# Performance work log

Measured on AMD Instinct MI355X. Metric: run time of the kernel, lower is better.

Reference implementation:

```python
import jax, jax.numpy as jnp
import numpy as np

IS, OS, H = 168, 24, 256           # input window, output horizon, state_hsize
TAU, MAXIMUM = 0.1, 1.0            # tau parameter (non-grad) and series maximum
DILS = [[1, 4], [16, 64]]          # ResidualDRNN groups of dilations


def _lstm(x, wih, whh, bih, bhh):
    """Single-layer LSTM over time-major x: (T, B, C). PyTorch gate order i,f,g,o."""
    def step(carry, xt):
        h, c = carry
        g = xt @ wih.T + h @ whh.T + (bih + bhh)
        i, f, gg, o = jnp.split(g, 4, axis=-1)
        c = jax.nn.sigmoid(f) * c + jax.nn.sigmoid(i) * jnp.tanh(gg)
        h = jax.nn.sigmoid(o) * jnp.tanh(c)
        return (h, c), h
    h0 = jnp.zeros((x.shape[1], H), x.dtype)
    _, hs = jax.lax.scan(step, (h0, h0), x)
    return hs


def _dilated_lstm(x, d, p):
    """Standard DRNN layer: pad T to multiple of d, interleave time into batch, run LSTM."""
    T, B, C = x.shape
    n = -(-T // d)
    xp = jnp.pad(x, ((0, n * d - T), (0, 0), (0, 0)))
    hd = _lstm(xp.reshape(n, d * B, C), *p)
    return hd.reshape(n * d, B, H)[:T]


def _forward(train, init_lev_sm, lstm_params, nl_w, nl_b, sc_w, sc_b):
    B, T = train.shape
    a = jax.nn.sigmoid(init_lev_sm[0])            # lev_sms (idxs are all 0 -> same scalar)
    floor = TAU * MAXIMUM                          # tau * maximum
    # --- exponential-smoothing level recurrence (sequential) ---
    lev0 = jnp.maximum(train[:, 0], floor)
    def step(lev, xt):
        new = jnp.maximum(a * xt + (1.0 - a) * lev, floor)
        return new, new
    _, rest = jax.lax.scan(step, lev0, train[:, 1:].T)
    levs = jnp.concatenate([lev0[None], rest], axis=0).T   # [B, T]
    # --- windowed normalization ---
    w_idx = jnp.arange(IS - 1, T)                           # W = T - IS + 1 window ends
    in_win = train[:, (w_idx - IS + 1)[:, None] + jnp.arange(IS)[None, :]]
    in_win = (in_win / levs[:, w_idx][:, :, None]).transpose(1, 0, 2)    # [W, B, IS]
    o_idx = jnp.arange(IS - 1, T - OS)                      # W_out = T - OS - IS + 1
    out_win = train[:, (o_idx + 1)[:, None] + jnp.arange(OS)[None, :]]
    out_win = (out_win / levs[:, o_idx][:, :, None]).transpose(1, 0, 2)  # [W_out, B, OS]
    # --- ResidualDRNN stack on window_input[:-OS] (time-major: windows are the sequence) ---
    x = in_win[:-OS]
    li = 0
    for g, dils in enumerate(DILS):
        residual = x
        h = x
        for d in dils:
            h = _dilated_lstm(h, d, lstm_params[li])
            li += 1
        x = h + residual if g > 0 else h                    # dropout p=0 -> identity
    x = jnp.tanh(x @ nl_w.T + nl_b)                         # add_nl_layer
    pred = x @ sc_w.T + sc_b                                # scoring
    return pred, out_win


def setup_inputs() -> dict:
    key = jax.random.key(0)
    ks = list(jax.random.split(key, 32))
    B, T = 32, 1024
    inp = {
        "train": jax.random.uniform(ks[0], (B, T), jnp.float32, 0.05, 1.0),
        "val": jax.random.uniform(ks[1], (B, T), jnp.float32, 0.05, 1.0),
        "test": jax.random.uniform(ks[2], (B, T), jnp.float32, 0.05, 1.0),
        "idxs": jnp.zeros((B,), jnp.int32),
        "init_lev_sm": jnp.array([0.5], jnp.float32),
    }
    sizes = [IS, H, H, H]  # input feature size of each of the 4 DRNN layers
    k = 3
    s = 1.0 / np.sqrt(H)
    for i, cin in enumerate(sizes):
        inp[f"wih{i}"] = jax.random.uniform(ks[k], (4 * H, cin), jnp.float32, -s, s); k += 1
        inp[f"whh{i}"] = jax.random.uniform(ks[k], (4 * H, H), jnp.float32, -s, s); k += 1
        inp[f"bih{i}"] = jax.random.uniform(ks[k], (4 * H,), jnp.float32, -s, s); k += 1
        inp[f"bhh{i}"] = jax.random.uniform(ks[k], (4 * H,), jnp.float32, -s, s); k += 1
    inp["nl_w"] = jax.random.uniform(ks[k], (H, H), jnp.float32, -s, s); k += 1
    inp["nl_b"] = jnp.zeros((H,), jnp.float32)
    inp["sc_w"] = jax.random.uniform(ks[k], (OS, H), jnp.float32, -s, s); k += 1
    inp["sc_b"] = jnp.zeros((OS,), jnp.float32)
    return inp


def reference(train, val, test, idxs, init_lev_sm,
              wih0, whh0, bih0, bhh0, wih1, whh1, bih1, bhh1,
              wih2, whh2, bih2, bhh2, wih3, whh3, bih3, bhh3,
              nl_w, nl_b, sc_w, sc_b):
    lstm_params = [(wih0, whh0, bih0, bhh0), (wih1, whh1, bih1, bhh1),
                   (wih2, whh2, bih2, bhh2), (wih3, whh3, bih3, bhh3)]
    # training path (validating=False, testing=False): only `train` is used
    return _forward(train, init_lev_sm, lstm_params, nl_w, nl_b, sc_w, sc_b)
```

## Files before the change

kernel.cpp:

```cpp
#include <hip/hip_runtime.h>
#include <hip/hip_fp16.h>
#include <math.h>

#define TT 833
#define GDIM 1024

typedef _Float16 f16x8 __attribute__((ext_vector_type(8)));
typedef float    f32x4 __attribute__((ext_vector_type(4)));

#if __has_builtin(__builtin_amdgcn_rcpf)
__device__ __forceinline__ float frcp(float x){ return __builtin_amdgcn_rcpf(x); }
#else
__device__ __forceinline__ float frcp(float x){ return 1.f/x; }
#endif

#if __has_builtin(__builtin_amdgcn_sdot4)
__device__ __forceinline__ int sdot4(unsigned a, unsigned b, int c){
  return __builtin_amdgcn_sdot4((int)a, (int)b, c, false);
}
#else
__device__ __forceinline__ int sdot4(unsigned a, unsigned b, int c){
  int ai = (int)a, bi = (int)b;
  c += ((ai<<24)>>24)*((bi<<24)>>24);
  c += ((ai<<16)>>24)*((bi<<16)>>24);
  c += ((ai<<8)>>24)*((bi<<8)>>24);
  c += (ai>>24)*(bi>>24);
  return c;
}
#endif

__device__ __forceinline__ void lds_barrier(){
  asm volatile("s_waitcnt lgkmcnt(0)" ::: "memory");
  __builtin_amdgcn_s_barrier();
  __builtin_amdgcn_sched_barrier(0);
}


__global__ void levels_k(const float* __restrict__ train, const float* __restrict__ ism,
                         float* __restrict__ levs){
  int b = threadIdx.x;
  if (b >= 32) return;
  float a = 1.f/(1.f+expf(-ism[0]));
  const float4* tr4 = reinterpret_cast<const float4*>(train + b*1024);
  float4* lv4 = reinterpret_cast<float4*>(levs + b*1024);
  float lev = 0.f;
  for (int i = 0; i < 256; ++i){
    float4 v = tr4[i];
    float4 o;
    if (i == 0) o.x = lev = fmaxf(v.x, 0.1f);
    else        o.x = lev = fmaxf(fmaf(a, v.x, (1.f-a)*lev), 0.1f);
    o.y = lev = fmaxf(fmaf(a, v.y, (1.f-a)*lev), 0.1f);
    o.z = lev = fmaxf(fmaf(a, v.z, (1.f-a)*lev), 0.1f);
    o.w = lev = fmaxf(fmaf(a, v.w, (1.f-a)*lev), 0.1f);
    lv4[i] = o;
  }
}

__global__ void win_x_k(const float* __restrict__ train, const float* __restrict__ levs,
                        __half* __restrict__ x0){
  int idx = blockIdx.x*256 + threadIdx.x;
  int i = idx % 168;
  int r = idx / 168;
  int b = r & 31;
  int t = r >> 5;
  x0[idx] = __float2half(train[b*1024 + t + i] / levs[b*1024 + t + 167]);
}

__global__ void win_out_k(const float* __restrict__ train, const float* __restrict__ levs,
                          float* __restrict__ ow){
  int idx = blockIdx.x*256 + threadIdx.x;
  int o = idx % 24;
  int r = idx / 24;
  int b = r & 31;
  int t = r >> 5;
  ow[idx] = train[b*1024 + 168 + t + o] / levs[b*1024 + t + 167];
}

__global__ void permw_k(const float* __restrict__ wih, const float* __restrict__ bih,
                        const float* __restrict__ bhh, __half* __restrict__ wP,
                        float* __restrict__ bP, int K){
  int t = blockIdx.x;
  int g = ((t & 3) << 8) + (t >> 2);
  for (int k = threadIdx.x; k < K; k += 256)
    wP[(size_t)t*K + k] = __float2half(wih[(size_t)g*K + k]);
  if (threadIdx.x == 0) bP[t] = bih[g] + bhh[g];
}

__global__ void cvth_k(const float* __restrict__ s, __half* __restrict__ d, int n){
  int i = blockIdx.x*256 + threadIdx.x;
  if (i < n) d[i] = __float2half(s[i]);
}

__global__ void packq_k(const float* __restrict__ w, uint4* __restrict__ wq,
                        float* __restrict__ sc){
  int t = blockIdx.x*256 + threadIdx.x;
  if (t >= 1024) return;
  int g = ((t & 3) << 8) + (t >> 2);
  const float* row = w + (size_t)g*256;
  float amax = 0.f;
  for (int k = 0; k < 256; ++k) amax = fmaxf(amax, fabsf(row[k]));
  amax = fmaxf(amax, 1e-20f);
  float s = amax/127.f, inv = 127.f/amax;
  sc[t] = s;
  for (int k16 = 0; k16 < 16; ++k16){
    union { uint4 u; signed char b[16]; } r;
    #pragma unroll
    for (int j = 0; j < 16; ++j){
      float q = rintf(row[k16*16 + j]*inv);
      q = fminf(fmaxf(q, -127.f), 127.f);
      r.b[j] = (signed char)q;
    }
    wq[(size_t)k16*1024 + t] = r.u;
  }
}

__global__ __launch_bounds__(256) void proj_mfma(
    const _Float16* __restrict__ A, const _Float16* __restrict__ W,
    const float* __restrict__ b1,
    void* __restrict__ C, int Mout, int K, int N, int dil, int act, int outHalf)
{
  __shared__ _Float16 As[128*40];
  __shared__ _Float16 Bs[128*40];
  const int tid = threadIdx.x;
  const int lane = tid & 63;
  const int w = tid >> 6, wr = w >> 1, wc = w & 1;
  const int m0 = blockIdx.y << 7, n0 = blockIdx.x << 7;

  const int rowA = tid >> 1;
  int srcrow;
  {
    int m = m0 + rowA;
    if (dil == 0) srcrow = (m < Mout) ? m : -1;
    else {
      int rows = dil << 5;
      int j = m / rows;
      int q = m - j*rows;
      int t = j*dil + (q >> 5);
      srcrow = (t < TT) ? ((t << 5) + (q & 31)) : -1;
    }
  }
  const int halfsel = tid & 1;
  const int nrow = n0 + rowA;

  f32x4 acc[4][4];
  #pragma unroll
  for (int i = 0; i < 4; ++i)
    #pragma unroll
    for (int j = 0; j < 4; ++j) acc[i][j] = (f32x4){0.f,0.f,0.f,0.f};

  const int nkt = (K + 31) >> 5;
  for (int kt = 0; kt < nkt; ++kt){
    const int k0 = (kt << 5) + halfsel*16;
    {
      union { uint4 u[2]; _Float16 h[16]; } tmp;
      if (srcrow >= 0 && k0 + 16 <= K){
        const uint4* s = reinterpret_cast<const uint4*>(A + (size_t)srcrow*K + k0);
        tmp.u[0] = s[0]; tmp.u[1] = s[1];
      } else {
        const _Float16* s = (srcrow >= 0) ? A + (size_t)srcrow*K : nullptr;
        #pragma unroll
        for (int j = 0; j < 16; ++j){
          int kk = k0 + j;
          tmp.h[j] = (s && kk < K) ? s[kk] : (_Float16)0.f;
        }
      }
      uint4* dst = reinterpret_cast<uint4*>(&As[rowA*40 + halfsel*16]);
      dst[0] = tmp.u[0]; dst[1] = tmp.u[1];
    }
    {
      union { uint4 u[2]; _Float16 h[16]; } tmp;
      if (k0 + 16 <= K){
        const uint4* s = reinterpret_cast<const uint4*>(W + (size_t)nrow*K + k0);
        tmp.u[0] = s[0]; tmp.u[1] = s[1];
      } else {
        const _Float16* s = W + (size_t)nrow*K;
        #pragma unroll
        for (int j = 0; j < 16; ++j){
          int kk = k0 + j;
          tmp.h[j] = (kk < K) ? s[kk] : (_Float16)0.f;
        }
      }
      uint4* dst = reinterpret_cast<uint4*>(&Bs[rowA*40 + halfsel*16]);
      dst[0] = tmp.u[0]; dst[1] = tmp.u[1];
    }
    __syncthreads();
    {
      const int kg = lane >> 4, r16 = lane & 15;
      f16x8 af[4], bf[4];
      #pragma unroll
      for (int mi = 0; mi < 4; ++mi)
        af[mi] = *reinterpret_cast<const f16x8*>(&As[(wr*64 + mi*16 + r16)*40 + kg*8]);
      #pragma unroll
      for (int nj = 0; nj < 4; ++nj)
        bf[nj] = *reinterpret_cast<const f16x8*>(&Bs[(wc*64 + nj*16 + r16)*40 + kg*8]);
      #pragma unroll
      for (int mi = 0; mi < 4; ++mi)
        #pragma unroll
        for (int nj = 0; nj < 4; ++nj)
          acc[mi][nj] = __builtin_amdgcn_mfma_f32_16x16x32_f16(af[mi], bf[nj], acc[mi][nj], 0, 0, 0);
    }
    __syncthreads();
  }
  #pragma unroll
  for (int mi = 0; mi < 4; ++mi){
    #pragma unroll
    for (int p = 0; p < 4; ++p){
      int mrow = m0 + wr*64 + mi*16 + (lane >> 4)*4 + p;
      if (mrow >= Mout) continue;
      #pragma unroll
      for (int nj = 0; nj < 4; ++nj){
        int ncol = n0 + wc*64 + nj*16 + (lane & 15);
        float v = acc[mi][nj][p] + b1[ncol];
        if (act) v = tanhf(v);
        if (outHalf) reinterpret_cast<__half*>(C)[(size_t)mrow*N + ncol] = __float2half(v);
        else reinterpret_cast<float*>(C)[(size_t)mrow*N + ncol] = v;
      }
    }
  }
}

template<int NR>
__global__ __launch_bounds__(512, 1) void srecr2_k(
    const uint4* __restrict__ wq, const float* __restrict__ scale,
    const __half* __restrict__ Gin,
    __half* __restrict__ outh, float* __restrict__ outf,
    int nsteps, int d, int rowsTotal)
{
  __shared__ __align__(16) unsigned int hq[2][NR][64];
  const int tid = threadIdx.x;
  const int s = tid & 1;
  const int j = tid >> 1;
  const int q0 = blockIdx.x*NR;
  const float sg0 = scale[2*tid]*(1.f/127.f);
  const float sg1 = scale[2*tid + 1]*(1.f/127.f);
  uint4 w0_[16], w1_[16];
  #pragma unroll
  for (int kk = 0; kk < 16; ++kk){
    w0_[kk] = wq[(size_t)kk*1024 + 2*tid];
    w1_[kk] = wq[(size_t)kk*1024 + 2*tid + 1];
  }
  float c[NR];
  #pragma unroll
  for (int rr = 0; rr < NR; ++rr) c[rr] = 0.f;
  for (int e = tid; e < 2*NR*64; e += 512) (&hq[0][0][0])[e] = 0u;
  __syncthreads();

  for (int step = 0; step < nsteps; ++step){
    const int cur = step & 1;
    const __half2* gbase = reinterpret_cast<const __half2*>(
        Gin + ((size_t)step*rowsTotal + q0)*GDIM);
    #pragma unroll
    for (int rr = 0; rr < NR; ++rr){
      __half2 g2 = gbase[rr*512 + tid];
      float gin0 = __half2float(__low2half(g2));
      float gin1 = __half2float(__high2half(g2));
      int a00 = 0, a01 = 0, a10 = 0, a11 = 0;
      #pragma unroll
      for (int k16 = 0; k16 < 8; ++k16){
        uint4 ha = *reinterpret_cast<const uint4*>(&hq[cur][rr][4*k16]);
        a00 = sdot4(w0_[k16].x, ha.x, a00); a00 = sdot4(w0_[k16].y, ha.y, a00);
        a00 = sdot4(w0_[k16].z, ha.z, a00); a00 = sdot4(w0_[k16].w, ha.w, a00);
        a10 = sdot4(w1_[k16].x, ha.x, a10); a10 = sdot4(w1_[k16].y, ha.y, a10);
        a10 = sdot4(w1_[k16].z, ha.z, a10); a10 = sdot4(w1_[k16].w, ha.w, a10);
        uint4 hb = *reinterpret_cast<const uint4*>(&hq[cur][rr][4*(k16 + 8)]);
        a01 = sdot4(w0_[k16+8].x, hb.x, a01); a01 = sdot4(w0_[k16+8].y, hb.y, a01);
        a01 = sdot4(w0_[k16+8].z, hb.z, a01); a01 = sdot4(w0_[k16+8].w, hb.w, a01);
        a11 = sdot4(w1_[k16+8].x, hb.x, a11); a11 = sdot4(w1_[k16+8].y, hb.y, a11);
        a11 = sdot4(w1_[k16+8].z, hb.z, a11); a11 = sdot4(w1_[k16+8].w, hb.w, a11);
      }
      float p0 = fmaf((float)(a00 + a01), sg0, gin0);
      float p1 = fmaf((float)(a10 + a11), sg1, gin1);
      float px0 = s ? p0 + p0 : p0;
      float t0 = frcp(1.f + __expf(-px0));
      float a0v = s ? fmaf(2.f, t0, -1.f) : t0;
      float a1v = frcp(1.f + __expf(-p1));
      float b0 = __shfl_xor(a0v, 1);
      float b1 = __shfl_xor(a1v, 1);
      float iv = s ? b0 : a0v;
      float fv = s ? b1 : a1v;
      float gv = s ? a0v : b0;
      float ov = s ? a1v : b1;
      float cn = fmaf(fv, c[rr], iv*gv);
      c[rr] = cn;
      if (s == 0){
        float e2 = __expf(-2.f*cn);
        float h = ov*(1.f - e2)*frcp(1.f + e2);
        int qh = (int)rintf(h*127.f);
        reinterpret_cast<signed char*>(&hq[cur^1][rr][0])[j] = (signed char)qh;
        int q = q0 + rr;
        int tg = step*d + (q >> 5);
        if (tg < TT){
          size_t oi = ((size_t)tg*32 + (q & 31))*256 + j;
          outh[oi] = __float2half(h);
          if (outf) outf[oi] = h;
        }
      }
    }
    lds_barrier();
  }
}

template<int NR>
__global__ __launch_bounds__(1024) void srecq_k(
    const uint4* __restrict__ wq, const float* __restrict__ scale,
    const __half* __restrict__ Gin,
    __half* __restrict__ outh, const float* __restrict__ res,
    int nsteps, int d, int rowsTotal)
{
  __shared__ __align__(16) unsigned int hq[2][NR][64];
  const int tid = threadIdx.x;
  const int lane = tid & 63;
  const int base = lane & ~3;
  const int kg = tid & 3;
  const int j = tid >> 2;
  const int q0 = blockIdx.x*NR;
  const float sg = scale[tid]*(1.f/127.f);
  float c[NR];
  #pragma unroll
  for (int rr = 0; rr < NR; ++rr) c[rr] = 0.f;
  for (int e = tid; e < 2*NR*64; e += 1024) (&hq[0][0][0])[e] = 0u;
  __syncthreads();

  for (int step = 0; step < nsteps; ++step){
    const int cur = step & 1;
    float gin[NR];
    const __half* gbase = Gin + ((size_t)step*rowsTotal + q0)*GDIM;
    #pragma unroll
    for (int rr = 0; rr < NR; ++rr) gin[rr] = __half2float(gbase[rr*GDIM + tid]);
    int acc[NR];
    #pragma unroll
    for (int rr = 0; rr < NR; ++rr) acc[rr] = 0;
    #pragma unroll 4
    for (int k16 = 0; k16 < 16; ++k16){
      uint4 w = wq[(size_t)k16*1024 + tid];
      #pragma unroll
      for (int rr = 0; rr < NR; ++rr){
        uint4 h4 = *reinterpret_cast<const uint4*>(&hq[cur][rr][4*k16]);
        acc[rr] = sdot4(w.x, h4.x, acc[rr]);
        acc[rr] = sdot4(w.y, h4.y, acc[rr]);
        acc[rr] = sdot4(w.z, h4.z, acc[rr]);
        acc[rr] = sdot4(w.w, h4.w, acc[rr]);
      }
    }
    #pragma unroll
    for (int rr = 0; rr < NR; ++rr){
      float p = fmaf((float)acc[rr], sg, gin[rr]);
      float px = (kg == 2) ? p + p : p;
      float sv = frcp(1.f + __expf(-px));
      float a = (kg == 2) ? fmaf(2.f, sv, -1.f) : sv;
      float iv = __shfl(a, base + 0);
      float fv = __shfl(a, base + 1);
      float gv = __shfl(a, base + 2);
      float ov = __shfl(a, base + 3);
      float cn = fmaf(fv, c[rr], iv*gv);
      c[rr] = cn;
      float e2 = __expf(-2.f*cn);
      float h = ov*(1.f - e2)*frcp(1.f + e2);
      if (kg == 0){
        int qh = (int)rintf(h*127.f);
        reinterpret_cast<signed char*>(&hq[cur^1][rr][0])[j] = (signed char)qh;
        int q = q0 + rr;
        int tg = step*d + (q >> 5);
        if (tg < TT){
          size_t oi = ((size_t)tg*32 + (q & 31))*256 + j;
          outh[oi] = __float2half(h + res[oi]);
        }
      }
    }
    lds_barrier();
  }
}

__global__ __launch_bounds__(256) void sc_head(const __half* __restrict__ xt, const float* __restrict__ w,
                        const float* __restrict__ bias, float* __restrict__ outp, int M){
  __shared__ float arow[8][256];
  int m0 = blockIdx.x << 3;
  int tid = threadIdx.x;
  #pragma unroll
  for (int i = 0; i < 8; ++i){
    int e = tid + (i << 8);
    int r = e >> 8, k = e & 255;
    arow[r][k] = (m0 + r < M) ? __half2float(xt[(size_t)(m0 + r)*256 + k]) : 0.f;
  }
  __syncthreads();
  int r = tid >> 5, n = tid & 31;
  if (n < 24 && (m0 + r) < M){
    float acc = bias[n];
    const float* wr = w + n*256;
    #pragma unroll 8
    for (int k = 0; k < 256; ++k) acc = fmaf(arow[r][k], wr[k], acc);
    outp[(size_t)(m0 + r)*24 + n] = acc;
  }
}

extern "C" void kernel_launch(void* const* d_in, const int* in_sizes, int n_in,
                              void* d_out, int out_size, void* d_ws, size_t ws_size,
                              hipStream_t stream){
  const float* train = (const float*)d_in[0];
  const float* ism   = (const float*)d_in[4];
  const float* wih[4] = {(const float*)d_in[5], (const float*)d_in[9], (const float*)d_in[13], (const float*)d_in[17]};
  const float* whh[4] = {(const float*)d_in[6], (const float*)d_in[10], (const float*)d_in[14], (const float*)d_in[18]};
  const float* bih[4] = {(const float*)d_in[7], (const float*)d_in[11], (const float*)d_in[15], (const float*)d_in[19]};
  const float* bhh[4] = {(const float*)d_in[8], (const float*)d_in[12], (const float*)d_in[16], (const float*)d_in[20]};
  const float* nl_w = (const float*)d_in[21];
  const float* nl_b = (const float*)d_in[22];
  const float* sc_w = (const float*)d_in[23];
  const float* sc_b = (const float*)d_in[24];
  float* out = (float*)d_out;

  float* ws = (float*)d_ws;
  size_t off = 0;
  float* levs = ws + off;   off += 32768;
  uint4* wqk[4];
  for (int l = 0; l < 4; ++l){ wqk[l] = (uint4*)(ws + off); off += 65536; }
  float* sck[4];
  for (int l = 0; l < 4; ++l){ sck[l] = ws + off; off += 1024; }
  __half* wPh[4];
  for (int l = 0; l < 4; ++l){ wPh[l] = (__half*)(ws + off); off += 131072; }
  float* bP[4];
  for (int l = 0; l < 4; ++l){ bP[l] = ws + off; off += 1024; }
  __half* nlwh = (__half*)(ws + off); off += 32768;
  __half* x0h = (__half*)(ws + off);  off += (size_t)26656*168/2;
  __half* G   = (__half*)(ws + off);  off += (size_t)28672*1024/2;
  __half* h0h = (__half*)(ws + off);  off += (size_t)26656*256/2;
  __half* h1h = (__half*)(ws + off);  off += (size_t)26656*256/2;
  float*  h1f = ws + off;             off += (size_t)26656*256;
  __half* h2h = (__half*)(ws + off);  off += (size_t)26656*256/2;
  __half* xfh = (__half*)(ws + off);  off += (size_t)26656*256/2;
  __half* xth = (__half*)(ws + off);  off += (size_t)26656*256/2;
  (void)ws_size; (void)in_sizes; (void)n_in; (void)out_size;

  levels_k<<<1, 64, 0, stream>>>(train, ism, levs);
  win_x_k<<<17493, 256, 0, stream>>>(train, levs, x0h);
  win_out_k<<<2499, 256, 0, stream>>>(train, levs, out + 639744);
  const int Kin[4] = {168, 256, 256, 256};
  for (int l = 0; l < 4; ++l){
    packq_k<<<4, 256, 0, stream>>>(whh[l], wqk[l], sck[l]);
    permw_k<<<1024, 256, 0, stream>>>(wih[l], bih[l], bhh[l], wPh[l], bP[l], Kin[l]);
  }
  cvth_k<<<256, 256, 0, stream>>>(nl_w, nlwh, 65536);

  proj_mfma<<<dim3(8,209), 256, 0, stream>>>((const _Float16*)x0h, (const _Float16*)wPh[0], bP[0], G, 26656, 168, 1024, 0, 0, 1);
  srecr2_k<1><<<32, 512, 0, stream>>>(wqk[0], sck[0], G, h0h, nullptr, 833, 1, 32);
  proj_mfma<<<dim3(8,209), 256, 0, stream>>>((const _Float16*)h0h, (const _Float16*)wPh[1], bP[1], G, 26752, 256, 1024, 4, 0, 1);
  srecr2_k<1><<<128, 512, 0, stream>>>(wqk[1], sck[1], G, h1h, h1f, 209, 4, 128);
  proj_mfma<<<dim3(8,212), 256, 0, stream>>>((const _Float16*)h1h, (const _Float16*)wPh[2], bP[2], G, 27136, 256, 1024, 16, 0, 1);
  srecr2_k<2><<<256, 512, 0, stream>>>(wqk[2], sck[2], G, h2h, nullptr, 53, 16, 512);
  proj_mfma<<<dim3(8,224), 256, 0, stream>>>((const _Float16*)h2h, (const _Float16*)wPh[3], bP[3], G, 28672, 256, 1024, 64, 0, 1);
  srecq_k<8><<<256, 1024, 0, stream>>>(wqk[3], sck[3], G, xfh, h1f, 14, 64, 2048);
  proj_mfma<<<dim3(2,209), 256, 0, stream>>>((const _Float16*)xfh, (const _Float16*)nlwh, nl_b, xth, 26656, 256, 256, 0, 1, 1);
  sc_head<<<3332, 256, 0, stream>>>(xth, sc_w, sc_b, out, 26656);
}
```

Before: 1.659 ms.

## Load MFMA operands directly from global memory and pad layer-0 K to 192

Replaces the LDS-staged GEMM with a version where each lane loads its f16x8 MFMA fragments straight from global memory. This removes the shared-memory staging and both barriers per k-step. The layer-0 input windows and input weights are zero-padded from 168 to 192 columns so every k-step is a full aligned 32-wide tile with no tail handling. In exchange there is no operand reuse through LDS, global loads are strided 16-byte accesses, and the padding adds a small amount of extra work and memory.

```diff
diff --git a/kernel.cpp b/kernel.cpp
--- a/kernel.cpp
+++ b/kernel.cpp
@@ -59,11 +59,12 @@
 __global__ void win_x_k(const float* __restrict__ train, const float* __restrict__ levs,
                         __half* __restrict__ x0){
   int idx = blockIdx.x*256 + threadIdx.x;
-  int i = idx % 168;
-  int r = idx / 168;
+  int i = idx % 192;
+  int r = idx / 192;
   int b = r & 31;
   int t = r >> 5;
-  x0[idx] = __float2half(train[b*1024 + t + i] / levs[b*1024 + t + 167]);
+  x0[idx] = (i < 168) ? __float2half(train[b*1024 + t + i] / levs[b*1024 + t + 167])
+                      : __float2half(0.f);
 }
 
 __global__ void win_out_k(const float* __restrict__ train, const float* __restrict__ levs,
@@ -78,11 +79,11 @@
 
 __global__ void permw_k(const float* __restrict__ wih, const float* __restrict__ bih,
                         const float* __restrict__ bhh, __half* __restrict__ wP,
-                        float* __restrict__ bP, int K){
+                        float* __restrict__ bP, int K, int Kpad){
   int t = blockIdx.x;
   int g = ((t & 3) << 8) + (t >> 2);
-  for (int k = threadIdx.x; k < K; k += 256)
-    wP[(size_t)t*K + k] = __float2half(wih[(size_t)g*K + k]);
+  for (int k = threadIdx.x; k < Kpad; k += 256)
+    wP[(size_t)t*Kpad + k] = (k < K) ? __float2half(wih[(size_t)g*K + k]) : __float2half(0.f);
   if (threadIdx.x == 0) bP[t] = bih[g] + bhh[g];
 }
 
@@ -114,33 +115,36 @@
   }
 }
 
-__global__ __launch_bounds__(256) void proj_mfma(
+__global__ __launch_bounds__(256) void proj_direct(
     const _Float16* __restrict__ A, const _Float16* __restrict__ W,
     const float* __restrict__ b1,
     void* __restrict__ C, int Mout, int K, int N, int dil, int act, int outHalf)
 {
-  __shared__ _Float16 As[128*40];
-  __shared__ _Float16 Bs[128*40];
   const int tid = threadIdx.x;
   const int lane = tid & 63;
   const int w = tid >> 6, wr = w >> 1, wc = w & 1;
   const int m0 = blockIdx.y << 7, n0 = blockIdx.x << 7;
-
-  const int rowA = tid >> 1;
-  int srcrow;
-  {
-    int m = m0 + rowA;
-    if (dil == 0) srcrow = (m < Mout) ? m : -1;
+  const int kg = lane >> 4, r16 = lane & 15;
+
+  int srow[4];
+  #pragma unroll
+  for (int mi = 0; mi < 4; ++mi){
+    int m = m0 + wr*64 + mi*16 + r16;
+    int row;
+    if (dil == 0) row = (m < Mout) ? m : -1;
     else {
       int rows = dil << 5;
-      int j = m / rows;
-      int q = m - j*rows;
-      int t = j*dil + (q >> 5);
-      srcrow = (t < TT) ? ((t << 5) + (q & 31)) : -1;
-    }
-  }
-  const int halfsel = tid & 1;
-  const int nrow = n0 + rowA;
+      int jj = m / rows;
+      int q = m - jj*rows;
+      int t = jj*dil + (q >> 5);
+      row = (t < TT) ? ((t << 5) + (q & 31)) : -1;
+    }
+    srow[mi] = row;
+  }
+  const _Float16* wbase[4];
+  #pragma unroll
+  for (int nj = 0; nj < 4; ++nj)
+    wbase[nj] = W + (size_t)(n0 + wc*64 + nj*16 + r16)*K;
 
   f32x4 acc[4][4];
   #pragma unroll
@@ -148,58 +152,25 @@
     #pragma unroll
     for (int j = 0; j < 4; ++j) acc[i][j] = (f32x4){0.f,0.f,0.f,0.f};
 
-  const int nkt = (K + 31) >> 5;
+  const int nkt = K >> 5;
+  #pragma unroll 2
   for (int kt = 0; kt < nkt; ++kt){
-    const int k0 = (kt << 5) + halfsel*16;
-    {
-      union { uint4 u[2]; _Float16 h[16]; } tmp;
-      if (srcrow >= 0 && k0 + 16 <= K){
-        const uint4* s = reinterpret_cast<const uint4*>(A + (size_t)srcrow*K + k0);
-        tmp.u[0] = s[0]; tmp.u[1] = s[1];
-      } else {
-        const _Float16* s = (srcrow >= 0) ? A + (size_t)srcrow*K : nullptr;
-        #pragma unroll
-        for (int j = 0; j < 16; ++j){
-          int kk = k0 + j;
-          tmp.h[j] = (s && kk < K) ? s[kk] : (_Float16)0.f;
-        }
-      }
-      uint4* dst = reinterpret_cast<uint4*>(&As[rowA*40 + halfsel*16]);
-      dst[0] = tmp.u[0]; dst[1] = tmp.u[1];
-    }
-    {
-      union { uint4 u[2]; _Float16 h[16]; } tmp;
-      if (k0 + 16 <= K){
-        const uint4* s = reinterpret_cast<const uint4*>(W + (size_t)nrow*K + k0);
-        tmp.u[0] = s[0]; tmp.u[1] = s[1];
-      } else {
-        const _Float16* s = W + (size_t)nrow*K;
-        #pragma unroll
-        for (int j = 0; j < 16; ++j){
-          int kk = k0 + j;
-          tmp.h[j] = (kk < K) ? s[kk] : (_Float16)0.f;
-        }
-      }
-      uint4* dst = reinterpret_cast<uint4*>(&Bs[rowA*40 + halfsel*16]);
-      dst[0] = tmp.u[0]; dst[1] = tmp.u[1];
-    }
-    __syncthreads();
-    {
-      const int kg = lane >> 4, r16 = lane & 15;
-      f16x8 af[4], bf[4];
-      #pragma unroll
-      for (int mi = 0; mi < 4; ++mi)
-        af[mi] = *reinterpret_cast<const f16x8*>(&As[(wr*64 + mi*16 + r16)*40 + kg*8]);
+    const int k = (kt << 5) + kg*8;
+    f16x8 af[4], bf[4];
+    #pragma unroll
+    for (int mi = 0; mi < 4; ++mi){
+      af[mi] = (f16x8){0,0,0,0,0,0,0,0};
+      if (srow[mi] >= 0)
+        af[mi] = *reinterpret_cast<const f16x8*>(A + (size_t)srow[mi]*K + k);
+    }
+    #pragma unroll
+    for (int nj = 0; nj < 4; ++nj)
+      bf[nj] = *reinterpret_cast<const f16x8*>(wbase[nj] + k);
+    #pragma unroll
+    for (int mi = 0; mi < 4; ++mi)
       #pragma unroll
       for (int nj = 0; nj < 4; ++nj)
-        bf[nj] = *reinterpret_cast<const f16x8*>(&Bs[(wc*64 + nj*16 + r16)*40 + kg*8]);
-      #pragma unroll
-      for (int mi = 0; mi < 4; ++mi)
-        #pragma unroll
-        for (int nj = 0; nj < 4; ++nj)
-          acc[mi][nj] = __builtin_amdgcn_mfma_f32_16x16x32_f16(af[mi], bf[nj], acc[mi][nj], 0, 0, 0);
-    }
-    __syncthreads();
+        acc[mi][nj] = __builtin_amdgcn_mfma_f32_16x16x32_f16(af[mi], bf[nj], acc[mi][nj], 0, 0, 0);
   }
   #pragma unroll
   for (int mi = 0; mi < 4; ++mi){
@@ -420,7 +391,7 @@
   float* bP[4];
   for (int l = 0; l < 4; ++l){ bP[l] = ws + off; off += 1024; }
   __half* nlwh = (__half*)(ws + off); off += 32768;
-  __half* x0h = (__half*)(ws + off);  off += (size_t)26656*168/2;
+  __half* x0h = (__half*)(ws + off);  off += (size_t)26656*192/2;
   __half* G   = (__half*)(ws + off);  off += (size_t)28672*1024/2;
   __half* h0h = (__half*)(ws + off);  off += (size_t)26656*256/2;
   __half* h1h = (__half*)(ws + off);  off += (size_t)26656*256/2;
@@ -431,23 +402,24 @@
   (void)ws_size; (void)in_sizes; (void)n_in; (void)out_size;
 
   levels_k<<<1, 64, 0, stream>>>(train, ism, levs);
-  win_x_k<<<17493, 256, 0, stream>>>(train, levs, x0h);
+  win_x_k<<<19992, 256, 0, stream>>>(train, levs, x0h);
   win_out_k<<<2499, 256, 0, stream>>>(train, levs, out + 639744);
-  const int Kin[4] = {168, 256, 256, 256};
+  const int Kin[4]  = {168, 256, 256, 256};
+  const int Kpad[4] = {192, 256, 256, 256};
   for (int l = 0; l < 4; ++l){
     packq_k<<<4, 256, 0, stream>>>(whh[l], wqk[l], sck[l]);
-    permw_k<<<1024, 256, 0, stream>>>(wih[l], bih[l], bhh[l], wPh[l], bP[l], Kin[l]);
+    permw_k<<<1024, 256, 0, stream>>>(wih[l], bih[l], bhh[l], wPh[l], bP[l], Kin[l], Kpad[l]);
   }
   cvth_k<<<256, 256, 0, stream>>>(nl_w, nlwh, 65536);
 
-  proj_mfma<<<dim3(8,209), 256, 0, stream>>>((const _Float16*)x0h, (const _Float16*)wPh[0], bP[0], G, 26656, 168, 1024, 0, 0, 1);
+  proj_direct<<<dim3(8,209), 256, 0, stream>>>((const _Float16*)x0h, (const _Float16*)wPh[0], bP[0], G, 26656, 192, 1024, 0, 0, 1);
   srecr2_k<1><<<32, 512, 0, stream>>>(wqk[0], sck[0], G, h0h, nullptr, 833, 1, 32);
-  proj_mfma<<<dim3(8,209), 256, 0, stream>>>((const _Float16*)h0h, (const _Float16*)wPh[1], bP[1], G, 26752, 256, 1024, 4, 0, 1);
+  proj_direct<<<dim3(8,209), 256, 0, stream>>>((const _Float16*)h0h, (const _Float16*)wPh[1], bP[1], G, 26752, 256, 1024, 4, 0, 1);
   srecr2_k<1><<<128, 512, 0, stream>>>(wqk[1], sck[1], G, h1h, h1f, 209, 4, 128);
-  proj_mfma<<<dim3(8,212), 256, 0, stream>>>((const _Float16*)h1h, (const _Float16*)wPh[2], bP[2], G, 27136, 256, 1024, 16, 0, 1);
+  proj_direct<<<dim3(8,212), 256, 0, stream>>>((const _Float16*)h1h, (const _Float16*)wPh[2], bP[2], G, 27136, 256, 1024, 16, 0, 1);
   srecr2_k<2><<<256, 512, 0, stream>>>(wqk[2], sck[2], G, h2h, nullptr, 53, 16, 512);
-  proj_mfma<<<dim3(8,224), 256, 0, stream>>>((const _Float16*)h2h, (const _Float16*)wPh[3], bP[3], G, 28672, 256, 1024, 64, 0, 1);
+  proj_direct<<<dim3(8,224), 256, 0, stream>>>((const _Float16*)h2h, (const _Float16*)wPh[3], bP[3], G, 28672, 256, 1024, 64, 0, 1);
   srecq_k<8><<<256, 1024, 0, stream>>>(wqk[3], sck[3], G, xfh, h1f, 14, 64, 2048);
-  proj_mfma<<<dim3(2,209), 256, 0, stream>>>((const _Float16*)xfh, (const _Float16*)nlwh, nl_b, xth, 26656, 256, 256, 0, 1, 1);
+  proj_direct<<<dim3(2,209), 256, 0, stream>>>((const _Float16*)xfh, (const _Float16*)nlwh, nl_b, xth, 26656, 256, 256, 0, 1, 1);
   sc_head<<<3332, 256, 0, stream>>>(xth, sc_w, sc_b, out, 26656);
 }
```

New measurement: 1.761 ms. +6.2%, slower.
